# Performance work log

Hardware: AMD Instinct MI355X
Metric: run time of the kernel (lower is better)

The kernel has to match this reference:

```python
import jax, jax.numpy as jnp
import numpy as np

NEG_INF = -1.0e9
LN_EPS = 1e-5
LEAK = 0.2


def setup_inputs() -> dict:
    key = jax.random.key(0)
    ks = jax.random.split(key, 8)
    B, C, T, N, H = 8, 64, 24, 512, 2
    hd = C // H
    x = jax.random.normal(ks[0], (B, C, T, N), dtype=jnp.float32)
    gso = jax.random.randint(ks[1], (N, N), 0, 2, dtype=jnp.int32)
    # torch nn.Linear weights are (out, in); xavier-ish scale
    s = (2.0 / (C + C)) ** 0.5
    Wq = jax.random.normal(ks[2], (C, C), dtype=jnp.float32) * s
    Wk = jax.random.normal(ks[3], (C, C), dtype=jnp.float32) * s
    Wv = jax.random.normal(ks[4], (C, C), dtype=jnp.float32) * s
    sa = (2.0 / (H + hd)) ** 0.5
    a_src = jax.random.normal(ks[5], (H, hd), dtype=jnp.float32) * sa
    a_dst = jax.random.normal(ks[6], (H, hd), dtype=jnp.float32) * sa
    ln_gamma = jnp.ones((C,), dtype=jnp.float32)
    ln_beta = jnp.zeros((C,), dtype=jnp.float32)
    return {"x": x, "gso": gso, "Wq": Wq, "Wk": Wk, "Wv": Wv,
            "a_src": a_src, "a_dst": a_dst, "ln_gamma": ln_gamma, "ln_beta": ln_beta}


def _spatial_gat(x, gso, Wq, Wk, Wv, a_src, a_dst, ln_gamma, ln_beta):
    B, C, T, N = x.shape
    H, hd = a_src.shape
    # (B, C, T, N) -> (B*T, N, C)
    xr = jnp.transpose(x, (0, 2, 3, 1)).reshape(B * T, N, C)
    # torch Linear: y = x @ W.T
    Q = jnp.einsum('bnc,dc->bnd', xr, Wq).reshape(B * T, N, H, hd)
    K = jnp.einsum('bnc,dc->bnd', xr, Wk).reshape(B * T, N, H, hd)
    V = jnp.einsum('bnc,dc->bnd', xr, Wv).reshape(B * T, N, H, hd)
    # additive GAT scores, all heads at once
    s_src = jnp.einsum('bnhd,hd->bnh', Q, a_src)  # (BT, N, H)
    s_dst = jnp.einsum('bnhd,hd->bnh', K, a_dst)  # (BT, N, H)
    scores = jax.nn.leaky_relu(s_src[:, :, None, :] + s_dst[:, None, :, :], LEAK)  # (BT, Ni, Nj, H)
    mask = jnp.where(gso == 0, jnp.float32(NEG_INF), jnp.float32(0.0))  # (N, N)
    scores = scores + mask[None, :, :, None]
    attn = jax.nn.softmax(scores, axis=2)  # softmax over destination j
    out = jnp.einsum('bijh,bjhd->bihd', attn, V)  # (BT, N, H, hd)
    out = out.reshape(B * T, N, C)
    # LayerNorm over channel dim
    mu = jnp.mean(out, axis=-1, keepdims=True)
    var = jnp.var(out, axis=-1, keepdims=True)
    out = (out - mu) * jax.lax.rsqrt(var + LN_EPS) * ln_gamma + ln_beta
    # back to (B, C, T, N)
    return jnp.transpose(out.reshape(B, T, N, C), (0, 3, 1, 2))


def reference(x, gso, Wq, Wk, Wv, a_src, a_dst, ln_gamma, ln_beta):
    return _spatial_gat(x, gso, Wq, Wk, Wv, a_src, a_dst, ln_gamma, ln_beta)
```

## Files before the change

kernel.cpp:

```cpp
#include <hip/hip_runtime.h>

#define CDIM 64
#define TDIM 24
#define NDIM 512
#define NBT  192

typedef float    float4v __attribute__((ext_vector_type(4)));
typedef _Float16 half8v  __attribute__((ext_vector_type(8)));
typedef _Float16 half4v  __attribute__((ext_vector_type(4)));
typedef _Float16 half2v  __attribute__((ext_vector_type(2)));


__device__ __forceinline__ float exp2_fast(float x) {
#if __has_builtin(__builtin_amdgcn_exp2f)
  return __builtin_amdgcn_exp2f(x);
#else
  return __expf(x * 0.69314718f);
#endif
}

struct SmemK1 {
  union {
    _Float16 xt[128][72];
    _Float16 vtb[64][136];
  } big;
  _Float16 wv[64][72];
  _Float16 wext[16][72];
};

__launch_bounds__(256, 4)
__global__ void k1_v(const float* __restrict__ x,  const float* __restrict__ Wv,
                     const float* __restrict__ Wq, const float* __restrict__ Wk,
                     const float* __restrict__ a_src, const float* __restrict__ a_dst,
                     const int* __restrict__ gso,
                     _Float16* __restrict__ VT_g,
                     float* __restrict__ s_src_g, float* __restrict__ s_dst_g,
                     unsigned char* __restrict__ maskb) {
  const int t  = threadIdx.x;
  const int bx = blockIdx.x;

  if (bx >= 768) {
    int g = (bx - 768) * 256 + t;
    const int4* gp = (const int4*)gso + (size_t)g * 4;
    unsigned w[4];
#pragma unroll
    for (int k = 0; k < 4; ++k) {
      int4 v = gp[k];
      w[k] = (v.x ? 0x000000FFu : 0u) | (v.y ? 0x0000FF00u : 0u) |
             (v.z ? 0x00FF0000u : 0u) | (v.w ? 0xFF000000u : 0u);
    }
    uint4 o; o.x = w[0]; o.y = w[1]; o.z = w[2]; o.w = w[3];
    ((uint4*)maskb)[g] = o;
    return;
  }

  __shared__ SmemK1 sm;
  const int qn = bx & 3;
  const int bt = bx >> 2;
  const int b  = bt / TDIM, tt = bt % TDIM;
  const int n0 = qn * 128;

#pragma unroll
  for (int it = 0; it < 4; ++it) {
    int idx = it * 256 + t;
    float4 vv = ((const float4*)Wv)[idx];
    int d = idx >> 4, k4 = (idx & 15) * 4;
    half4v h4; h4[0] = (_Float16)vv.x; h4[1] = (_Float16)vv.y;
    h4[2] = (_Float16)vv.z; h4[3] = (_Float16)vv.w;
    *(half4v*)&sm.wv[d][k4] = h4;
  }
  for (int z = t; z < 12 * 72; z += 256) ((_Float16*)sm.wext[4])[z] = (_Float16)0.f;
  if (t < 64) {
    int c = t;
    float s0 = 0.f, s1 = 0.f, d0 = 0.f, d1 = 0.f;
#pragma unroll
    for (int d = 0; d < 32; ++d) {
      s0 += a_src[d]      * Wq[d * 64 + c];
      s1 += a_src[32 + d] * Wq[(32 + d) * 64 + c];
      d0 += a_dst[d]      * Wk[d * 64 + c];
      d1 += a_dst[32 + d] * Wk[(32 + d) * 64 + c];
    }
    const float l2e = 1.44269504f;
    sm.wext[0][c] = (_Float16)(s0 * l2e); sm.wext[1][c] = (_Float16)(s1 * l2e);
    sm.wext[2][c] = (_Float16)(d0 * l2e); sm.wext[3][c] = (_Float16)(d1 * l2e);
  }
  for (int it = 0; it < 16; ++it) {
    int idx = it * 256 + t;
    int cp = idx >> 7, n = idx & 127;
    int c0 = cp * 2;
    const float* base = x + ((size_t)(b * CDIM + c0) * TDIM + tt) * NDIM + n0 + n;
    half2v p; p[0] = (_Float16)base[0]; p[1] = (_Float16)base[(size_t)TDIM * NDIM];
    *(half2v*)&sm.big.xt[n][c0] = p;
  }
  __syncthreads();

  const int lane = t & 63, w = t >> 6;
  const int m = lane & 15, quad = lane >> 4;
  const int mbase = w * 32;

  float4v acc[2][5];
#pragma unroll
  for (int mt = 0; mt < 2; ++mt)
#pragma unroll
    for (int nt = 0; nt < 5; ++nt)
#pragma unroll
      for (int r = 0; r < 4; ++r) acc[mt][nt][r] = 0.f;

#pragma unroll
  for (int ks = 0; ks < 2; ++ks) {
    half8v af[2], bf[5];
#pragma unroll
    for (int mt = 0; mt < 2; ++mt)
      af[mt] = *(const half8v*)&sm.big.xt[mbase + mt * 16 + m][ks * 32 + quad * 8];
#pragma unroll
    for (int nt = 0; nt < 4; ++nt)
      bf[nt] = *(const half8v*)&sm.wv[nt * 16 + m][ks * 32 + quad * 8];
    bf[4] = *(const half8v*)&sm.wext[m][ks * 32 + quad * 8];
#pragma unroll
    for (int mt = 0; mt < 2; ++mt)
#pragma unroll
      for (int nt = 0; nt < 5; ++nt)
        acc[mt][nt] = __builtin_amdgcn_mfma_f32_16x16x32_f16(af[mt], bf[nt], acc[mt][nt], 0, 0, 0);
  }

  if (m < 4) {
    float* basep = (m < 2 ? s_src_g : s_dst_g) + (size_t)(bt * 2 + (m & 1)) * NDIM;
#pragma unroll
    for (int mt = 0; mt < 2; ++mt)
#pragma unroll
      for (int r = 0; r < 4; ++r)
        basep[n0 + mbase + mt * 16 + quad * 4 + r] = acc[mt][4][r];
  }
  __syncthreads();

#pragma unroll
  for (int mt = 0; mt < 2; ++mt)
#pragma unroll
    for (int nt = 0; nt < 4; ++nt)
#pragma unroll
      for (int r = 0; r < 4; r += 2) {
        int nl = mbase + mt * 16 + quad * 4 + r;
        int c  = nt * 16 + m;
        half2v p = __builtin_bit_cast(half2v,
            __builtin_amdgcn_cvt_pkrtz(acc[mt][nt][r], acc[mt][nt][r + 1]));
        *(half2v*)&sm.big.vtb[c][nl] = p;
      }
  __syncthreads();

  const uint4* vq = (const uint4*)sm.big.vtb;
#pragma unroll
  for (int it = 0; it < 4; ++it) {
    int idx = it * 256 + t;
    int c = idx >> 4, q4 = idx & 15;
    ((uint4*)VT_g)[(size_t)(bt * 64 + c) * 64 + qn * 16 + q4] = vq[c * 17 + q4];
  }
}

struct SmemK2 {
  union {
    struct { _Float16 vt[64][128]; } s;
    struct { float otile[128][66]; float rsum[2][128]; float rsq[2][128];
             float mu[128]; float rs[128]; } e;
  } u;
  _Float16 sF16[2][512];
  _Float16 sP16[2][512];
};

__launch_bounds__(256, 3)
__global__ void k2_attn(const _Float16* __restrict__ VT_g,
                        const float* __restrict__ s_src_g, const float* __restrict__ s_dst_g,
                        const unsigned char* __restrict__ maskb,
                        const float* __restrict__ gamma, const float* __restrict__ beta,
                        float* __restrict__ out) {
  __shared__ SmemK2 sm;
  const int t     = threadIdx.x;
  const int id    = blockIdx.x;
  const int itile = (id >> 3) & 3;
  const int bt    = ((id >> 5) << 3) | (id & 7);
  const int i0    = itile * 128;
  const int b     = bt / TDIM, tt = bt % TDIM;
  const int lane  = t & 63, w = t >> 6;
  const int h = w >> 1, ihalf = w & 1;
  const int m = lane & 15, quad = lane >> 4;
  const int rbase = ihalf * 64;

  for (int it = 0; it < 4; ++it) {
    int idx = it * 256 + t;
    float d = s_dst_g[(size_t)bt * 2 * NDIM + idx];
    ((_Float16*)sm.sF16)[idx] = (_Float16)exp2_fast(d);
    ((_Float16*)sm.sP16)[idx] = (_Float16)exp2_fast(0.2f * d);
  }
  half2v e2[4], q2[4];
#pragma unroll
  for (int mt = 0; mt < 4; ++mt) {
    float sv = s_src_g[(size_t)(bt * 2 + h) * NDIM + i0 + rbase + mt * 16 + m];
    _Float16 ev = (_Float16)exp2_fast(sv - 6.f);
    _Float16 qv = (_Float16)exp2_fast(0.2f * sv - 6.f);
    e2[mt][0] = ev; e2[mt][1] = ev;
    q2[mt][0] = qv; q2[mt][1] = qv;
  }

  float4v acc[4][2], accs[4];
#pragma unroll
  for (int mt = 0; mt < 4; ++mt)
#pragma unroll
    for (int r = 0; r < 4; ++r) { acc[mt][0][r] = 0.f; acc[mt][1][r] = 0.f; accs[mt][r] = 0.f; }
  const half8v bones = {(_Float16)1.f, (_Float16)1.f, (_Float16)1.f, (_Float16)1.f,
                        (_Float16)1.f, (_Float16)1.f, (_Float16)1.f, (_Float16)1.f};

  const uint4* vsrc = (const uint4*)VT_g;
  uint4 pv0, pv1, pv2, pv3;
  const int vc  = t >> 4;
  const int vch = t & 15;
  const int vswz = (vch * 8) ^ ((vc & 7) * 8);

  const unsigned char* mrow = maskb + (size_t)(i0 + rbase + m) * NDIM + quad * 8;

#define PREFETCH(js_)                                                          \
  {                                                                            \
    pv0 = vsrc[(size_t)(bt * 64 + vc     ) * 64 + (js_) * 16 + vch];           \
    pv1 = vsrc[(size_t)(bt * 64 + vc + 16) * 64 + (js_) * 16 + vch];           \
    pv2 = vsrc[(size_t)(bt * 64 + vc + 32) * 64 + (js_) * 16 + vch];           \
    pv3 = vsrc[(size_t)(bt * 64 + vc + 48) * 64 + (js_) * 16 + vch];           \
  }

  PREFETCH(0);

#pragma unroll
  for (int js = 0; js < 4; ++js) {
    __syncthreads();
    *(uint4*)&sm.u.s.vt[vc     ][vswz] = pv0;
    *(uint4*)&sm.u.s.vt[vc + 16][vswz] = pv1;
    *(uint4*)&sm.u.s.vt[vc + 32][vswz] = pv2;
    *(uint4*)&sm.u.s.vt[vc + 48][vswz] = pv3;
    __syncthreads();
    if (js < 3) PREFETCH(js + 1);

    uint2 mk[4][4];
#pragma unroll
    for (int mt = 0; mt < 4; ++mt) {
      const unsigned char* mbp = mrow + (size_t)(mt * 16) * NDIM + js * 128;
#pragma unroll
      for (int ksl = 0; ksl < 4; ++ksl)
        mk[mt][ksl] = *(const uint2*)(mbp + ksl * 32);
    }

#pragma unroll
    for (int ksl = 0; ksl < 4; ++ksl) {
      int jq = ksl * 32 + quad * 8;
      half8v F8 = *(const half8v*)&sm.sF16[h][js * 128 + jq];
      half8v P8 = *(const half8v*)&sm.sP16[h][js * 128 + jq];
      int vbase = (h * 32 + m) * 128 + (jq ^ ((m & 7) * 8));
      half8v b0 = *(const half8v*)&sm.u.s.vt[0][vbase];
      half8v b1 = *(const half8v*)&sm.u.s.vt[0][vbase + 16 * 128];
      uint4 fu = __builtin_bit_cast(uint4, F8);
      uint4 pu = __builtin_bit_cast(uint4, P8);
      half2v f2a = __builtin_bit_cast(half2v, fu.x), f2b = __builtin_bit_cast(half2v, fu.y);
      half2v f2c = __builtin_bit_cast(half2v, fu.z), f2d = __builtin_bit_cast(half2v, fu.w);
      half2v p2a = __builtin_bit_cast(half2v, pu.x), p2b = __builtin_bit_cast(half2v, pu.y);
      half2v p2c = __builtin_bit_cast(half2v, pu.z), p2d = __builtin_bit_cast(half2v, pu.w);
#pragma unroll
      for (int mt = 0; mt < 4; ++mt) {
        unsigned mw0 = mk[mt][ksl].x, mw1 = mk[mt][ksl].y;
        uint4 eu;
        eu.x = __builtin_bit_cast(unsigned,
                 __builtin_elementwise_max(e2[mt] * f2a, q2[mt] * p2a)) &
               __builtin_amdgcn_perm(0u, mw0, 0x01010000u);
        eu.y = __builtin_bit_cast(unsigned,
                 __builtin_elementwise_max(e2[mt] * f2b, q2[mt] * p2b)) &
               __builtin_amdgcn_perm(0u, mw0, 0x03030202u);
        eu.z = __builtin_bit_cast(unsigned,
                 __builtin_elementwise_max(e2[mt] * f2c, q2[mt] * p2c)) &
               __builtin_amdgcn_perm(0u, mw1, 0x01010000u);
        eu.w = __builtin_bit_cast(unsigned,
                 __builtin_elementwise_max(e2[mt] * f2d, q2[mt] * p2d)) &
               __builtin_amdgcn_perm(0u, mw1, 0x03030202u);
        half8v af = __builtin_bit_cast(half8v, eu);
        acc[mt][0] = __builtin_amdgcn_mfma_f32_16x16x32_f16(af, b0,    acc[mt][0], 0, 0, 0);
        acc[mt][1] = __builtin_amdgcn_mfma_f32_16x16x32_f16(af, b1,    acc[mt][1], 0, 0, 0);
        accs[mt]   = __builtin_amdgcn_mfma_f32_16x16x32_f16(af, bones, accs[mt],   0, 0, 0);
      }
    }
  }
#undef PREFETCH

  __syncthreads();
#pragma unroll
  for (int mt = 0; mt < 4; ++mt)
#pragma unroll
    for (int r = 0; r < 4; ++r) {
      float sc = __builtin_amdgcn_rcpf(accs[mt][r]);
      int i_loc = rbase + mt * 16 + quad * 4 + r;
#pragma unroll
      for (int nt = 0; nt < 2; ++nt)
        sm.u.e.otile[i_loc][h * 32 + nt * 16 + m] = acc[mt][nt][r] * sc;
    }
  __syncthreads();

  {
    int i = t & 127, cg = t >> 7;
    float s1 = 0.f, s2 = 0.f;
#pragma unroll
    for (int cc = 0; cc < 32; ++cc) {
      float v = sm.u.e.otile[i][cg * 32 + cc];
      s1 += v; s2 += v * v;
    }
    sm.u.e.rsum[cg][i] = s1;
    sm.u.e.rsq[cg][i]  = s2;
  }
  __syncthreads();
  if (t < 128) {
    int i = t;
    float s1 = sm.u.e.rsum[0][i] + sm.u.e.rsum[1][i];
    float s2 = sm.u.e.rsq[0][i]  + sm.u.e.rsq[1][i];
    float mu  = s1 * (1.f / 64.f);
    float var = s2 * (1.f / 64.f) - mu * mu;
    sm.u.e.mu[i] = mu;
    sm.u.e.rs[i] = rsqrtf(var + 1e-5f);
  }
  __syncthreads();
  {
    int i = t & 127, cg = t >> 7;
    float mu = sm.u.e.mu[i], rs = sm.u.e.rs[i];
    int n = i0 + i;
#pragma unroll
    for (int cc = 0; cc < 32; ++cc) {
      int c = cg * 32 + cc;
      float v = (sm.u.e.otile[i][c] - mu) * rs * gamma[c] + beta[c];
      out[((size_t)(b * CDIM + c) * TDIM + tt) * NDIM + n] = v;
    }
  }
}

extern "C" void kernel_launch(void* const* d_in, const int* in_sizes, int n_in,
                              void* d_out, int out_size, void* d_ws, size_t ws_size,
                              hipStream_t stream) {
  const float* x     = (const float*)d_in[0];
  const int*   gso   = (const int*)d_in[1];
  const float* Wq    = (const float*)d_in[2];
  const float* Wk    = (const float*)d_in[3];
  const float* Wv    = (const float*)d_in[4];
  const float* a_src = (const float*)d_in[5];
  const float* a_dst = (const float*)d_in[6];
  const float* gamma = (const float*)d_in[7];
  const float* beta  = (const float*)d_in[8];
  float* out = (float*)d_out;

  char* ws = (char*)d_ws;
  _Float16* VT_g  = (_Float16*)ws;
  float*    s_src = (float*)(ws + 12582912);
  float*    s_dst = (float*)(ws + 13369344);
  unsigned char* maskb = (unsigned char*)(ws + 14155776);

  k1_v<<<832, 256, 0, stream>>>(x, Wv, Wq, Wk, a_src, a_dst, gso,
                                VT_g, s_src, s_dst, maskb);
  k2_attn<<<768, 256, 0, stream>>>(VT_g, s_src, s_dst, maskb, gamma, beta, out);
}
```

Baseline: 121.7 us.

## Precompute exp2 score factors in producer kernel and split V prefetch across slices

Moves the exp2 of source/destination scores from the attention kernel into the projection kernel, storing fp16 factor arrays instead of fp32 scores. This removes exp work repeated by every i-tile block and halves the score traffic. The V-tile prefetch is split in two halves issued at different points in the slice loop to spread register pressure, and k2's launch bounds are raised to 4 blocks per CU. The higher occupancy target may force register spills.

Result: no change. 122.8 us (+0.9%).

```diff
diff --git a/kernel.cpp b/kernel.cpp
--- a/kernel.cpp
+++ b/kernel.cpp
@@ -34,7 +34,8 @@
                      const float* __restrict__ a_src, const float* __restrict__ a_dst,
                      const int* __restrict__ gso,
                      _Float16* __restrict__ VT_g,
-                     float* __restrict__ s_src_g, float* __restrict__ s_dst_g,
+                     _Float16* __restrict__ F16, _Float16* __restrict__ P16,
+                     _Float16* __restrict__ E16, _Float16* __restrict__ Q16,
                      unsigned char* __restrict__ maskb) {
   const int t  = threadIdx.x;
   const int bx = blockIdx.x;
@@ -124,12 +125,20 @@
   }
 
   if (m < 4) {
-    float* basep = (m < 2 ? s_src_g : s_dst_g) + (size_t)(bt * 2 + (m & 1)) * NDIM;
+    const int hh = m & 1;
+    const bool is_src = (m < 2);
+    _Float16* eb = (is_src ? E16 : F16) + ((size_t)(bt * 2 + hh)) * NDIM;
+    _Float16* qb = (is_src ? Q16 : P16) + ((size_t)(bt * 2 + hh)) * NDIM;
+    const float bias = is_src ? -6.f : 0.f;
 #pragma unroll
     for (int mt = 0; mt < 2; ++mt)
 #pragma unroll
-      for (int r = 0; r < 4; ++r)
-        basep[n0 + mbase + mt * 16 + quad * 4 + r] = acc[mt][4][r];
+      for (int r = 0; r < 4; ++r) {
+        float s = acc[mt][4][r];
+        int n = n0 + mbase + mt * 16 + quad * 4 + r;
+        eb[n] = (_Float16)exp2_fast(s + bias);
+        qb[n] = (_Float16)exp2_fast(0.2f * s + bias);
+      }
   }
   __syncthreads();
 
@@ -166,9 +175,10 @@
   _Float16 sP16[2][512];
 };
 
-__launch_bounds__(256, 3)
+__launch_bounds__(256, 4)
 __global__ void k2_attn(const _Float16* __restrict__ VT_g,
-                        const float* __restrict__ s_src_g, const float* __restrict__ s_dst_g,
+                        const _Float16* __restrict__ F16, const _Float16* __restrict__ P16,
+                        const _Float16* __restrict__ E16, const _Float16* __restrict__ Q16,
                         const unsigned char* __restrict__ maskb,
                         const float* __restrict__ gamma, const float* __restrict__ beta,
                         float* __restrict__ out) {
@@ -184,20 +194,23 @@
   const int m = lane & 15, quad = lane >> 4;
   const int rbase = ihalf * 64;
 
-  for (int it = 0; it < 4; ++it) {
-    int idx = it * 256 + t;
-    float d = s_dst_g[(size_t)bt * 2 * NDIM + idx];
-    ((_Float16*)sm.sF16)[idx] = (_Float16)exp2_fast(d);
-    ((_Float16*)sm.sP16)[idx] = (_Float16)exp2_fast(0.2f * d);
+  {
+    uint2 fv = ((const uint2*)(F16 + (size_t)bt * 2 * NDIM))[t];
+    uint2 pw = ((const uint2*)(P16 + (size_t)bt * 2 * NDIM))[t];
+    ((uint2*)sm.sF16)[t] = fv;
+    ((uint2*)sm.sP16)[t] = pw;
   }
   half2v e2[4], q2[4];
-#pragma unroll
-  for (int mt = 0; mt < 4; ++mt) {
-    float sv = s_src_g[(size_t)(bt * 2 + h) * NDIM + i0 + rbase + mt * 16 + m];
-    _Float16 ev = (_Float16)exp2_fast(sv - 6.f);
-    _Float16 qv = (_Float16)exp2_fast(0.2f * sv - 6.f);
-    e2[mt][0] = ev; e2[mt][1] = ev;
-    q2[mt][0] = qv; q2[mt][1] = qv;
+  {
+    const _Float16* eb = E16 + ((size_t)(bt * 2 + h)) * NDIM + i0 + rbase + m;
+    const _Float16* qb = Q16 + ((size_t)(bt * 2 + h)) * NDIM + i0 + rbase + m;
+#pragma unroll
+    for (int mt = 0; mt < 4; ++mt) {
+      _Float16 ev = eb[mt * 16];
+      _Float16 qv = qb[mt * 16];
+      e2[mt][0] = ev; e2[mt][1] = ev;
+      q2[mt][0] = qv; q2[mt][1] = qv;
+    }
   }
 
   float4v acc[4][2], accs[4];
@@ -216,15 +229,52 @@
 
   const unsigned char* mrow = maskb + (size_t)(i0 + rbase + m) * NDIM + quad * 8;
 
-#define PREFETCH(js_)                                                          \
+#define PREFETCH_A(js_)                                                        \
+  { pv0 = vsrc[(size_t)(bt * 64 + vc     ) * 64 + (js_) * 16 + vch];           \
+    pv1 = vsrc[(size_t)(bt * 64 + vc + 16) * 64 + (js_) * 16 + vch]; }
+#define PREFETCH_B(js_)                                                        \
+  { pv2 = vsrc[(size_t)(bt * 64 + vc + 32) * 64 + (js_) * 16 + vch];           \
+    pv3 = vsrc[(size_t)(bt * 64 + vc + 48) * 64 + (js_) * 16 + vch]; }
+
+#define SLICE(js_, ksl_)                                                       \
   {                                                                            \
-    pv0 = vsrc[(size_t)(bt * 64 + vc     ) * 64 + (js_) * 16 + vch];           \
-    pv1 = vsrc[(size_t)(bt * 64 + vc + 16) * 64 + (js_) * 16 + vch];           \
-    pv2 = vsrc[(size_t)(bt * 64 + vc + 32) * 64 + (js_) * 16 + vch];           \
-    pv3 = vsrc[(size_t)(bt * 64 + vc + 48) * 64 + (js_) * 16 + vch];           \
-  }
-
-  PREFETCH(0);
+    const int jq = (ksl_) * 32 + quad * 8;                                     \
+    half8v F8 = *(const half8v*)&sm.sF16[h][(js_) * 128 + jq];                 \
+    half8v P8 = *(const half8v*)&sm.sP16[h][(js_) * 128 + jq];                 \
+    const int vbase = (h * 32 + m) * 128 + (jq ^ ((m & 7) * 8));               \
+    half8v b0 = *(const half8v*)&sm.u.s.vt[0][vbase];                          \
+    half8v b1 = *(const half8v*)&sm.u.s.vt[0][vbase + 16 * 128];               \
+    uint4 fu = __builtin_bit_cast(uint4, F8);                                  \
+    uint4 pu = __builtin_bit_cast(uint4, P8);                                  \
+    half2v f2a = __builtin_bit_cast(half2v, fu.x), f2b = __builtin_bit_cast(half2v, fu.y); \
+    half2v f2c = __builtin_bit_cast(half2v, fu.z), f2d = __builtin_bit_cast(half2v, fu.w); \
+    half2v p2a = __builtin_bit_cast(half2v, pu.x), p2b = __builtin_bit_cast(half2v, pu.y); \
+    half2v p2c = __builtin_bit_cast(half2v, pu.z), p2d = __builtin_bit_cast(half2v, pu.w); \
+    _Pragma("unroll")                                                          \
+    for (int mt = 0; mt < 4; ++mt) {                                           \
+      unsigned mw0 = mk[mt][ksl_].x, mw1 = mk[mt][ksl_].y;                     \
+      uint4 eu;                                                                \
+      eu.x = __builtin_bit_cast(unsigned,                                      \
+               __builtin_elementwise_max(e2[mt] * f2a, q2[mt] * p2a)) &        \
+             __builtin_amdgcn_perm(0u, mw0, 0x01010000u);                      \
+      eu.y = __builtin_bit_cast(unsigned,                                      \
+               __builtin_elementwise_max(e2[mt] * f2b, q2[mt] * p2b)) &        \
+             __builtin_amdgcn_perm(0u, mw0, 0x03030202u);                      \
+      eu.z = __builtin_bit_cast(unsigned,                                      \
+               __builtin_elementwise_max(e2[mt] * f2c, q2[mt] * p2c)) &        \
+             __builtin_amdgcn_perm(0u, mw1, 0x01010000u);                      \
+      eu.w = __builtin_bit_cast(unsigned,                                      \
+               __builtin_elementwise_max(e2[mt] * f2d, q2[mt] * p2d)) &        \
+             __builtin_amdgcn_perm(0u, mw1, 0x03030202u);                      \
+      half8v af = __builtin_bit_cast(half8v, eu);                              \
+      acc[mt][0] = __builtin_amdgcn_mfma_f32_16x16x32_f16(af, b0,    acc[mt][0], 0, 0, 0); \
+      acc[mt][1] = __builtin_amdgcn_mfma_f32_16x16x32_f16(af, b1,    acc[mt][1], 0, 0, 0); \
+      accs[mt]   = __builtin_amdgcn_mfma_f32_16x16x32_f16(af, bones, accs[mt],   0, 0, 0); \
+    }                                                                          \
+  }
+
+  PREFETCH_A(0);
+  PREFETCH_B(0);
 
 #pragma unroll
   for (int js = 0; js < 4; ++js) {
@@ -234,7 +284,7 @@
     *(uint4*)&sm.u.s.vt[vc + 32][vswz] = pv2;
     *(uint4*)&sm.u.s.vt[vc + 48][vswz] = pv3;
     __syncthreads();
-    if (js < 3) PREFETCH(js + 1);
+    if (js < 3) PREFETCH_A(js + 1);
 
     uint2 mk[4][4];
 #pragma unroll
@@ -245,44 +295,15 @@
         mk[mt][ksl] = *(const uint2*)(mbp + ksl * 32);
     }
 
-#pragma unroll
-    for (int ksl = 0; ksl < 4; ++ksl) {
-      int jq = ksl * 32 + quad * 8;
-      half8v F8 = *(const half8v*)&sm.sF16[h][js * 128 + jq];
-      half8v P8 = *(const half8v*)&sm.sP16[h][js * 128 + jq];
-      int vbase = (h * 32 + m) * 128 + (jq ^ ((m & 7) * 8));
-      half8v b0 = *(const half8v*)&sm.u.s.vt[0][vbase];
-      half8v b1 = *(const half8v*)&sm.u.s.vt[0][vbase + 16 * 128];
-      uint4 fu = __builtin_bit_cast(uint4, F8);
-      uint4 pu = __builtin_bit_cast(uint4, P8);
-      half2v f2a = __builtin_bit_cast(half2v, fu.x), f2b = __builtin_bit_cast(half2v, fu.y);
-      half2v f2c = __builtin_bit_cast(half2v, fu.z), f2d = __builtin_bit_cast(half2v, fu.w);
-      half2v p2a = __builtin_bit_cast(half2v, pu.x), p2b = __builtin_bit_cast(half2v, pu.y);
-      half2v p2c = __builtin_bit_cast(half2v, pu.z), p2d = __builtin_bit_cast(half2v, pu.w);
-#pragma unroll
-      for (int mt = 0; mt < 4; ++mt) {
-        unsigned mw0 = mk[mt][ksl].x, mw1 = mk[mt][ksl].y;
-        uint4 eu;
-        eu.x = __builtin_bit_cast(unsigned,
-                 __builtin_elementwise_max(e2[mt] * f2a, q2[mt] * p2a)) &
-               __builtin_amdgcn_perm(0u, mw0, 0x01010000u);
-        eu.y = __builtin_bit_cast(unsigned,
-                 __builtin_elementwise_max(e2[mt] * f2b, q2[mt] * p2b)) &
-               __builtin_amdgcn_perm(0u, mw0, 0x03030202u);
-        eu.z = __builtin_bit_cast(unsigned,
-                 __builtin_elementwise_max(e2[mt] * f2c, q2[mt] * p2c)) &
-               __builtin_amdgcn_perm(0u, mw1, 0x01010000u);
-        eu.w = __builtin_bit_cast(unsigned,
-                 __builtin_elementwise_max(e2[mt] * f2d, q2[mt] * p2d)) &
-               __builtin_amdgcn_perm(0u, mw1, 0x03030202u);
-        half8v af = __builtin_bit_cast(half8v, eu);
-        acc[mt][0] = __builtin_amdgcn_mfma_f32_16x16x32_f16(af, b0,    acc[mt][0], 0, 0, 0);
-        acc[mt][1] = __builtin_amdgcn_mfma_f32_16x16x32_f16(af, b1,    acc[mt][1], 0, 0, 0);
-        accs[mt]   = __builtin_amdgcn_mfma_f32_16x16x32_f16(af, bones, accs[mt],   0, 0, 0);
-      }
-    }
-  }
-#undef PREFETCH
+    SLICE(js, 0);
+    SLICE(js, 1);
+    if (js < 3) PREFETCH_B(js + 1);
+    SLICE(js, 2);
+    SLICE(js, 3);
+  }
+#undef SLICE
+#undef PREFETCH_A
+#undef PREFETCH_B
 
   __syncthreads();
 #pragma unroll
@@ -347,12 +368,15 @@
   float* out = (float*)d_out;
 
   char* ws = (char*)d_ws;
-  _Float16* VT_g  = (_Float16*)ws;
-  float*    s_src = (float*)(ws + 12582912);
-  float*    s_dst = (float*)(ws + 13369344);
+  _Float16* VT_g = (_Float16*)ws;
+  _Float16* F16  = (_Float16*)(ws + 12582912);
+  _Float16* P16  = (_Float16*)(ws + 12976128);
+  _Float16* E16  = (_Float16*)(ws + 13369344);
+  _Float16* Q16  = (_Float16*)(ws + 13762560);
   unsigned char* maskb = (unsigned char*)(ws + 14155776);
 
   k1_v<<<832, 256, 0, stream>>>(x, Wv, Wq, Wk, a_src, a_dst, gso,
-                                VT_g, s_src, s_dst, maskb);
-  k2_attn<<<768, 256, 0, stream>>>(VT_g, s_src, s_dst, maskb, gamma, beta, out);
+                                VT_g, F16, P16, E16, Q16, maskb);
+  k2_attn<<<768, 256, 0, stream>>>(VT_g, F16, P16, E16, Q16, maskb,
+                                   gamma, beta, out);
 }
```
